# Kernel tuning notes

Hardware: AMD Instinct MI355X
Metric: run time of the kernel (lower is better)

The kernel has to match this reference:

```python
import jax, jax.numpy as jnp
import numpy as np

GAMMA = 2.0
EPS = 1e-12  # tf.nn.l2_normalize epsilon


def setup_inputs() -> dict:
    key = jax.random.key(0)
    k1, k2 = jax.random.split(key)
    B, H, W_, C = 8, 56, 56, 256
    x = jax.random.normal(k1, (B, H, W_, C), dtype=jnp.float32)
    W = jax.random.normal(k2, (C, C), dtype=jnp.float32) * 0.05
    return {"x": x, "W": W}


def reference(x, W):
    B, H, Wd, C = x.shape
    hw = H * Wd
    # transform branch: 1x1 conv, no bias (num_layers=1)
    t = jnp.einsum('bhwc,cd->bhwd', x, W).reshape(B, hw, C)
    # pixel affinity: cosine similarity (tf: -cosine_similarity == cos sim)
    xf = x.reshape(B, hw, C)
    inv_norm = jax.lax.rsqrt(jnp.maximum(jnp.sum(xf * xf, axis=-1, keepdims=True), EPS))
    xn = xf * inv_norm
    sim = jnp.einsum('bic,bjc->bij', xn, xn)  # [B, hw, hw]
    sim = jnp.power(jax.nn.relu(sim), GAMMA)
    y = jnp.einsum('bij,bjc->bic', sim, t)
    return y.reshape(B, H, Wd, C)
```

## Files before the change

kernel.cpp:

```cpp
#include <hip/hip_runtime.h>

#define HW 3136
#define CH 256
#define NJT 49
#define NIT 25
#define NPIX 25088

typedef __attribute__((ext_vector_type(8))) short bf16x8;
typedef __attribute__((ext_vector_type(4))) float f32x4;
typedef __attribute__((ext_vector_type(16))) float f32x16;
typedef unsigned short u16;
typedef unsigned int u32;

static __device__ __forceinline__ u16 f2bf(float f){
  union { float f; u32 u; } v; v.f = f;
  u32 r = v.u + 0x7FFFu + ((v.u >> 16) & 1u);
  return (u16)(r >> 16);
}

static __device__ __forceinline__ void gload16(const void* g, void* l){
  __builtin_amdgcn_global_load_lds(
      (const __attribute__((address_space(1))) unsigned int*)g,
      (__attribute__((address_space(3))) unsigned int*)l, 16, 0, 0);
}

static __device__ __forceinline__ f32x16 zero16(){
  f32x16 v;
  #pragma unroll
  for (int e = 0; e < 16; ++e) v[e] = 0.f;
  return v;
}

static __device__ __forceinline__ int ssw(int i, int c){
  return (((c + (i >> 3)) & 7) ^ (i & 7));
}

__global__ __launch_bounds__(256) void prep_wt(const float* __restrict__ W,
                                               u16* __restrict__ Wt){
  const int o = blockIdx.x, i = threadIdx.x;
  Wt[o*CH + i] = f2bf(W[i*CH + o]);
}

__global__ __launch_bounds__(256) void gemm_t(const float* __restrict__ x,
                                              const u16* __restrict__ Wt,
                                              u16* __restrict__ xn_bf,
                                              u16* __restrict__ tT){
  __shared__ u16 sT[256*64];
  const int jt = blockIdx.x, b = blockIdx.y;
  const int tid = threadIdx.x, wid = tid >> 6, lane = tid & 63;
  const int l15 = lane & 15, l4 = lane >> 4;
  const int j0 = jt * 64;
  const int row = j0 + wid*16 + l15;
  const float* xp = x + ((size_t)b*HW + row)*CH + l4*8;

  float xv[8][8];
  float ss = 0.f;
  #pragma unroll
  for (int kb = 0; kb < 8; ++kb){
    const float4 v0 = *(const float4*)(xp + kb*32);
    const float4 v1 = *(const float4*)(xp + kb*32 + 4);
    xv[kb][0]=v0.x; xv[kb][1]=v0.y; xv[kb][2]=v0.z; xv[kb][3]=v0.w;
    xv[kb][4]=v1.x; xv[kb][5]=v1.y; xv[kb][6]=v1.z; xv[kb][7]=v1.w;
    #pragma unroll
    for (int e = 0; e < 8; ++e) ss += xv[kb][e]*xv[kb][e];
  }
  ss += __shfl_xor(ss, 16);
  ss += __shfl_xor(ss, 32);
  const float inv = rsqrtf(fmaxf(ss, 1e-12f));

  bf16x8 ax[8];
  #pragma unroll
  for (int kb = 0; kb < 8; ++kb){
    bf16x8 a, n;
    #pragma unroll
    for (int e = 0; e < 8; ++e){
      a[e] = (short)f2bf(xv[kb][e]);
      n[e] = (short)f2bf(xv[kb][e]*inv);
    }
    ax[kb] = a;
    *(bf16x8*)(xn_bf + ((size_t)b*HW + row)*CH + kb*32 + l4*8) = n;
  }

  f32x4 acc[16];
  #pragma unroll
  for (int n = 0; n < 16; ++n) acc[n] = f32x4{0.f,0.f,0.f,0.f};
  #pragma unroll
  for (int kb = 0; kb < 8; ++kb){
    #pragma unroll
    for (int n0 = 0; n0 < 16; ++n0){
      const bf16x8 bb = *(const bf16x8*)(Wt + (n0*16 + l15)*CH + kb*32 + l4*8);
      acc[n0] = __builtin_amdgcn_mfma_f32_16x16x32_bf16(ax[kb], bb, acc[n0], 0, 0, 0);
    }
  }
  #pragma unroll
  for (int n0 = 0; n0 < 16; ++n0){
    const int c = n0*16 + l15;
    const int jloc = wid*16 + l4*4;
    const int gj = jloc >> 3;
    ushort4 w4;
    w4.x = f2bf(acc[n0][0]); w4.y = f2bf(acc[n0][1]);
    w4.z = f2bf(acc[n0][2]); w4.w = f2bf(acc[n0][3]);
    *(ushort4*)&sT[c*64 + ((gj ^ (c & 7)) * 8) + (jloc & 7)] = w4;
  }
  __syncthreads();
  #pragma unroll
  for (int p = 0; p < 8; ++p){
    const int c = p*32 + (tid >> 3);
    const int q = tid & 7;
    const bf16x8 v = *(const bf16x8*)&sT[c*64 + ((q ^ (c & 7)) * 8)];
    *(bf16x8*)(tT + ((size_t)b*CH + c)*HW + j0 + q*8) = v;
  }
}

__global__ __launch_bounds__(512) void ppm_main(const u16* __restrict__ xn,
                                                const u16* __restrict__ tT,
                                                float* __restrict__ out){
  __shared__ u16 sXJ[2][64*256];
  __shared__ u16 sTJ[2][256*64];
  __shared__ u16 sS [128*64];

  const int it = blockIdx.x, b = blockIdx.y;
  const int tid = threadIdx.x, wid = tid >> 6, lane = tid & 63;
  const int l31 = lane & 31, hi = lane >> 5;
  const int i0 = it * 128;
  const int wqj = wid >> 2, wqi = wid & 3;
  const int wpi = wid >> 2, wpc = wid & 3;

  bf16x8 aq[16];
  {
    int irow = i0 + wqi*32 + l31;
    if (irow >= HW) irow = HW - 1;
    const u16* p = xn + ((size_t)b*HW + irow)*CH + hi*8;
    #pragma unroll
    for (int kb = 0; kb < 16; ++kb) aq[kb] = *(const bf16x8*)(p + kb*16);
  }

  f32x16 accY[2][2];
  #pragma unroll
  for (int mi = 0; mi < 2; ++mi)
    #pragma unroll
    for (int ni = 0; ni < 2; ++ni) accY[mi][ni] = zero16();

  const size_t xbase = (size_t)b*HW;
  const size_t tbase = (size_t)b*CH;

  auto STAGE = [&](int buf, int jt){
    const int j0 = jt * 64;
    #pragma unroll
    for (int q = 0; q < 4; ++q){
      const int m = q*512 + tid;
      { const int row = m >> 5, g = m & 31;
        gload16(xn + (xbase + j0 + row)*CH + ((g ^ (row & 7)) * 8), &sXJ[buf][m*8]); }
      { const int c = m >> 3, g = m & 7;
        gload16(tT + (tbase + c)*HW + j0 + ((g ^ (c & 7)) * 8), &sTJ[buf][m*8]); }
    }
  };

  auto ITER = [&](int buf, int jt, bool stg){
    if (stg) STAGE(buf ^ 1, jt + 1);

    f32x16 sa = zero16(), sb = zero16();
    const int rj = wqj*32 + l31;
    const int rsw = rj & 7;
    #pragma unroll
    for (int kb = 0; kb < 16; kb += 2){
      const bf16x8 a0 = *(const bf16x8*)&sXJ[buf][rj*256 + (((kb*2 + hi)     ^ rsw) * 8)];
      const bf16x8 a1 = *(const bf16x8*)&sXJ[buf][rj*256 + (((kb*2 + 2 + hi) ^ rsw) * 8)];
      sa = __builtin_amdgcn_mfma_f32_32x32x16_bf16(a0, aq[kb],   sa, 0, 0, 0);
      sb = __builtin_amdgcn_mfma_f32_32x32x16_bf16(a1, aq[kb+1], sb, 0, 0, 0);
    }
    const int i_loc = wqi*32 + l31;
    #pragma unroll
    for (int q = 0; q < 4; ++q){
      ushort4 w4;
      #pragma unroll
      for (int r = 0; r < 4; ++r){
        float v = sa[q*4 + r] + sb[q*4 + r];
        v = fmaxf(v, 0.f);
        v *= v;
        ((u16*)&w4)[r] = f2bf(v);
      }
      const int jb = q*8 + hi*4;
      const int jl = wqj*32 + jb;
      *(ushort4*)&sS[i_loc*64 + ssw(i_loc, jl >> 3)*8 + (jb & 7)] = w4;
    }
    __syncthreads();

    #pragma unroll
    for (int kb = 0; kb < 4; ++kb){
      bf16x8 pa[2], pb[2];
      #pragma unroll
      for (int mi = 0; mi < 2; ++mi){
        const int i = wpi*64 + mi*32 + l31;
        pa[mi] = *(const bf16x8*)&sS[i*64 + ssw(i, kb*2 + hi)*8];
      }
      #pragma unroll
      for (int ni = 0; ni < 2; ++ni){
        const int c = wpc*64 + ni*32 + l31;
        pb[ni] = *(const bf16x8*)&sTJ[buf][c*64 + (((kb*2 + hi) ^ (c & 7)) * 8)];
      }
      #pragma unroll
      for (int mi = 0; mi < 2; ++mi)
        #pragma unroll
        for (int ni = 0; ni < 2; ++ni)
          accY[mi][ni] = __builtin_amdgcn_mfma_f32_32x32x16_bf16(pa[mi], pb[ni], accY[mi][ni], 0, 0, 0);
    }
    __syncthreads();
  };

  STAGE(0, 0);
  __syncthreads();

  #pragma unroll 1
  for (int jt = 0; jt < NJT - 1; jt += 2){
    ITER(0, jt,     true);
    ITER(1, jt + 1, jt + 2 < NJT);
  }
  ITER(0, NJT - 1, false);

  #pragma unroll
  for (int mi = 0; mi < 2; ++mi)
    #pragma unroll
    for (int ni = 0; ni < 2; ++ni)
      #pragma unroll
      for (int r = 0; r < 16; ++r){
        const int row = i0 + wpi*64 + mi*32 + (r & 3) + 8*(r >> 2) + 4*hi;
        if (row < HW)
          out[((size_t)b*HW + row)*CH + wpc*64 + ni*32 + l31] = accY[mi][ni][r];
      }
}

extern "C" void kernel_launch(void* const* d_in, const int* in_sizes, int n_in,
                              void* d_out, int out_size, void* d_ws, size_t ws_size,
                              hipStream_t stream){
  const float* x = (const float*)d_in[0];
  const float* W = (const float*)d_in[1];
  float* out = (float*)d_out;
  char* ws = (char*)d_ws;

  const size_t SZ = (size_t)NPIX * CH * sizeof(u16);
  u16* xn_bf = (u16*)(ws);
  u16* tT    = (u16*)(ws + SZ);
  u16* Wt    = (u16*)(ws + 2*SZ);

  prep_wt<<<CH, CH, 0, stream>>>(W, Wt);
  gemm_t<<<dim3(NJT, 8), 256, 0, stream>>>(x, Wt, xn_bf, tT);
  ppm_main<<<dim3(NIT, 8), 512, 0, stream>>>(xn_bf, tT, out);
}
```

Baseline: 156.5 us.

## Keep similarity tile in registers and split the PV GEMM across j-halves

Stops staging the relu-squared similarity tile through shared memory. Each wave packs its S fragment to bf16 with v_cvt_pk_bf16_f32 and uses permlane32_swap so it can serve directly as the MFMA B operand, with the wave accumulating its own j-slice across all 256 channels. The two j-half partial sums are then reduced through LDS at the end with coalesced float4 stores. This drops one __syncthreads and the sS round trip per tile, and adds s_setprio around the MFMA loops. In exchange each wave holds 8 f32x16 accumulators, which raises register pressure, and the epilogue now does an extra LDS reduction.

```diff
diff --git a/kernel.cpp b/kernel.cpp
--- a/kernel.cpp
+++ b/kernel.cpp
@@ -31,9 +31,7 @@
   return v;
 }
 
-static __device__ __forceinline__ int ssw(int i, int c){
-  return (((c + (i >> 3)) & 7) ^ (i & 7));
-}
+#define MFMA32(A,B,C) __builtin_amdgcn_mfma_f32_32x32x16_bf16((A),(B),(C),0,0,0)
 
 __global__ __launch_bounds__(256) void prep_wt(const float* __restrict__ W,
                                                u16* __restrict__ Wt){
@@ -115,16 +113,13 @@
 __global__ __launch_bounds__(512) void ppm_main(const u16* __restrict__ xn,
                                                 const u16* __restrict__ tT,
                                                 float* __restrict__ out){
-  __shared__ u16 sXJ[2][64*256];
-  __shared__ u16 sTJ[2][256*64];
-  __shared__ u16 sS [128*64];
+  __shared__ u16 SM[65536];
 
   const int it = blockIdx.x, b = blockIdx.y;
   const int tid = threadIdx.x, wid = tid >> 6, lane = tid & 63;
   const int l31 = lane & 31, hi = lane >> 5;
   const int i0 = it * 128;
   const int wqj = wid >> 2, wqi = wid & 3;
-  const int wpi = wid >> 2, wpc = wid & 3;
 
   bf16x8 aq[16];
   {
@@ -132,102 +127,137 @@
     if (irow >= HW) irow = HW - 1;
     const u16* p = xn + ((size_t)b*HW + irow)*CH + hi*8;
     #pragma unroll
-    for (int kb = 0; kb < 16; ++kb) aq[kb] = *(const bf16x8*)(p + kb*16);
-  }
-
-  f32x16 accY[2][2];
-  #pragma unroll
-  for (int mi = 0; mi < 2; ++mi)
-    #pragma unroll
-    for (int ni = 0; ni < 2; ++ni) accY[mi][ni] = zero16();
+    for (int ks = 0; ks < 16; ++ks) aq[ks] = *(const bf16x8*)(p + ks*16);
+  }
+
+  f32x16 accY[8];
+  #pragma unroll
+  for (int cb = 0; cb < 8; ++cb) accY[cb] = zero16();
 
   const size_t xbase = (size_t)b*HW;
   const size_t tbase = (size_t)b*CH;
 
-  auto STAGE = [&](int buf, int jt){
-    const int j0 = jt * 64;
+  {
+    u16* nXJ = SM;
+    u16* nTJ = SM + 16384;
     #pragma unroll
     for (int q = 0; q < 4; ++q){
       const int m = q*512 + tid;
       { const int row = m >> 5, g = m & 31;
-        gload16(xn + (xbase + j0 + row)*CH + ((g ^ (row & 7)) * 8), &sXJ[buf][m*8]); }
+        gload16(xn + (xbase + row)*CH + ((g ^ (row & 7))*8), &nXJ[m*8]); }
       { const int c = m >> 3, g = m & 7;
-        gload16(tT + (tbase + c)*HW + j0 + ((g ^ (c & 7)) * 8), &sTJ[buf][m*8]); }
-    }
-  };
-
-  auto ITER = [&](int buf, int jt, bool stg){
-    if (stg) STAGE(buf ^ 1, jt + 1);
+        gload16(tT + (tbase + c)*HW + ((g ^ (c & 7))*8), &nTJ[m*8]); }
+    }
+    __syncthreads();
+  }
+
+  #pragma unroll 1
+  for (int jt = 0; jt < NJT; ++jt){
+    const int buf = jt & 1;
+    u16* sXJ = SM + buf*32768;
+    u16* sTJ = sXJ + 16384;
+
+    if (jt + 1 < NJT){
+      u16* nXJ = SM + (buf ^ 1)*32768;
+      u16* nTJ = nXJ + 16384;
+      const int j0n = (jt + 1)*64;
+      #pragma unroll
+      for (int q = 0; q < 4; ++q){
+        const int m = q*512 + tid;
+        { const int row = m >> 5, g = m & 31;
+          gload16(xn + (xbase + j0n + row)*CH + ((g ^ (row & 7))*8), &nXJ[m*8]); }
+        { const int c = m >> 3, g = m & 7;
+          gload16(tT + (tbase + c)*HW + j0n + ((g ^ (c & 7))*8), &nTJ[m*8]); }
+      }
+    }
 
     f32x16 sa = zero16(), sb = zero16();
     const int rj = wqj*32 + l31;
     const int rsw = rj & 7;
-    #pragma unroll
-    for (int kb = 0; kb < 16; kb += 2){
-      const bf16x8 a0 = *(const bf16x8*)&sXJ[buf][rj*256 + (((kb*2 + hi)     ^ rsw) * 8)];
-      const bf16x8 a1 = *(const bf16x8*)&sXJ[buf][rj*256 + (((kb*2 + 2 + hi) ^ rsw) * 8)];
-      sa = __builtin_amdgcn_mfma_f32_32x32x16_bf16(a0, aq[kb],   sa, 0, 0, 0);
-      sb = __builtin_amdgcn_mfma_f32_32x32x16_bf16(a1, aq[kb+1], sb, 0, 0, 0);
-    }
-    const int i_loc = wqi*32 + l31;
-    #pragma unroll
-    for (int q = 0; q < 4; ++q){
-      ushort4 w4;
-      #pragma unroll
-      for (int r = 0; r < 4; ++r){
-        float v = sa[q*4 + r] + sb[q*4 + r];
-        v = fmaxf(v, 0.f);
-        v *= v;
-        ((u16*)&w4)[r] = f2bf(v);
-      }
-      const int jb = q*8 + hi*4;
-      const int jl = wqj*32 + jb;
-      *(ushort4*)&sS[i_loc*64 + ssw(i_loc, jl >> 3)*8 + (jb & 7)] = w4;
-    }
+    const u16* xjrow = &sXJ[rj*256];
+    __builtin_amdgcn_s_setprio(1);
+    #pragma unroll
+    for (int kb = 0; kb < 8; ++kb){
+      const bf16x8 a0 = *(const bf16x8*)&xjrow[(((kb*4 + hi)     ^ rsw) * 8)];
+      const bf16x8 a1 = *(const bf16x8*)&xjrow[(((kb*4 + 2 + hi) ^ rsw) * 8)];
+      sa = MFMA32(a0, aq[2*kb],   sa);
+      sb = MFMA32(a1, aq[2*kb+1], sb);
+    }
+    __builtin_amdgcn_s_setprio(0);
+
+    float s0,s1,s2,s3,s4,s5,s6,s7,s8,s9,s10,s11,s12,s13,s14,s15;
+#define SREL(d, r) { float v_ = sa[r] + sb[r]; v_ = fmaxf(v_, 0.f); d = v_ * v_; }
+    SREL(s0,0) SREL(s1,1) SREL(s2,2) SREL(s3,3) SREL(s4,4) SREL(s5,5) SREL(s6,6) SREL(s7,7)
+    SREL(s8,8) SREL(s9,9) SREL(s10,10) SREL(s11,11) SREL(s12,12) SREL(s13,13) SREL(s14,14) SREL(s15,15)
+#undef SREL
+    u32 w0,w1,w2,w3,w4,w5,w6,w7;
+#define PK(d, a, c) asm("v_cvt_pk_bf16_f32 %0, %1, %2" : "=v"(d) : "v"(a), "v"(c));
+    PK(w0, s0, s1)  PK(w1, s2, s3)  PK(w2, s4, s5)  PK(w3, s6, s7)
+    PK(w4, s8, s9)  PK(w5, s10,s11) PK(w6, s12,s13) PK(w7, s14,s15)
+#undef PK
+    asm volatile("v_permlane32_swap_b32 %0, %1" : "+v"(w0), "+v"(w2));
+    asm volatile("v_permlane32_swap_b32 %0, %1" : "+v"(w1), "+v"(w3));
+    asm volatile("v_permlane32_swap_b32 %0, %1" : "+v"(w4), "+v"(w6));
+    asm volatile("v_permlane32_swap_b32 %0, %1" : "+v"(w5), "+v"(w7));
+    union { u32 u[4]; bf16x8 v; } fb0, fb1;
+    fb0.u[0]=w0; fb0.u[1]=w1; fb0.u[2]=w2; fb0.u[3]=w3;
+    fb1.u[0]=w4; fb1.u[1]=w5; fb1.u[2]=w6; fb1.u[3]=w7;
+    const bf16x8 pb0 = fb0.v, pb1 = fb1.v;
+
+    __builtin_amdgcn_s_setprio(1);
+    #pragma unroll
+    for (int ks = 0; ks < 2; ++ks){
+      const bf16x8 pbk = ks ? pb1 : pb0;
+      #pragma unroll
+      for (int cb = 0; cb < 8; ++cb){
+        const int c = cb*32 + l31;
+        const bf16x8 af = *(const bf16x8*)&sTJ[c*64 + (((wqj*4 + ks*2 + hi) ^ (c & 7)) * 8)];
+        accY[cb] = MFMA32(af, pbk, accY[cb]);
+      }
+    }
+    __builtin_amdgcn_s_setprio(0);
+
     __syncthreads();
-
-    #pragma unroll
-    for (int kb = 0; kb < 4; ++kb){
-      bf16x8 pa[2], pb[2];
-      #pragma unroll
-      for (int mi = 0; mi < 2; ++mi){
-        const int i = wpi*64 + mi*32 + l31;
-        pa[mi] = *(const bf16x8*)&sS[i*64 + ssw(i, kb*2 + hi)*8];
-      }
-      #pragma unroll
-      for (int ni = 0; ni < 2; ++ni){
-        const int c = wpc*64 + ni*32 + l31;
-        pb[ni] = *(const bf16x8*)&sTJ[buf][c*64 + (((kb*2 + hi) ^ (c & 7)) * 8)];
-      }
-      #pragma unroll
-      for (int mi = 0; mi < 2; ++mi)
-        #pragma unroll
-        for (int ni = 0; ni < 2; ++ni)
-          accY[mi][ni] = __builtin_amdgcn_mfma_f32_32x32x16_bf16(pa[mi], pb[ni], accY[mi][ni], 0, 0, 0);
-    }
-    __syncthreads();
-  };
-
-  STAGE(0, 0);
+  }
+
+  float* Yl = (float*)SM;
+  const int il = wqi*32 + l31;
+  const int isw = (il & 7) << 2;
+  if (wqj == 0){
+    #pragma unroll
+    for (int cb = 0; cb < 8; ++cb)
+      #pragma unroll
+      for (int r = 0; r < 16; ++r){
+        const int c = cb*32 + (r & 3) + 8*(r >> 2) + 4*hi;
+        Yl[il*256 + (c ^ isw)] = accY[cb][r];
+      }
+  }
   __syncthreads();
-
-  #pragma unroll 1
-  for (int jt = 0; jt < NJT - 1; jt += 2){
-    ITER(0, jt,     true);
-    ITER(1, jt + 1, jt + 2 < NJT);
-  }
-  ITER(0, NJT - 1, false);
-
-  #pragma unroll
-  for (int mi = 0; mi < 2; ++mi)
-    #pragma unroll
-    for (int ni = 0; ni < 2; ++ni)
+  if (wqj == 1){
+    #pragma unroll
+    for (int cb = 0; cb < 8; ++cb)
       #pragma unroll
       for (int r = 0; r < 16; ++r){
-        const int row = i0 + wpi*64 + mi*32 + (r & 3) + 8*(r >> 2) + 4*hi;
-        if (row < HW)
-          out[((size_t)b*HW + row)*CH + wpc*64 + ni*32 + l31] = accY[mi][ni][r];
-      }
+        const int c = cb*32 + (r & 3) + 8*(r >> 2) + 4*hi;
+        const int idx = il*256 + (c ^ isw);
+        Yl[idx] += accY[cb][r];
+      }
+  }
+  __syncthreads();
+  {
+    const int i3 = tid >> 2;
+    const int cq = (tid & 3) * 64;
+    const int sw3 = (i3 & 7) << 2;
+    if (i0 + i3 < HW){
+      float* orow = out + ((size_t)b*HW + i0 + i3)*CH;
+      #pragma unroll
+      for (int q = 0; q < 16; ++q){
+        const int c = cq + q*4;
+        const float4 v = *(const float4*)&Yl[i3*256 + (c ^ sw3)];
+        *(float4*)&orow[c] = v;
+      }
+    }
+  }
 }
 
 extern "C" void kernel_launch(void* const* d_in, const int* in_sizes, int n_in,
```

Measured after the change: 221.7 us. 41.7% more time.
